# Optimization experiments

Hardware: AMD Instinct MI355X
Metric: run time of the kernel (lower is better)

## Reference

```python
import jax, jax.numpy as jnp
import numpy as np

B, T, D = 8, 1024, 768
H, HD = 12, 64
DFF = 3072
EPS = 1e-5


def setup_inputs() -> dict:
    key = jax.random.key(0)
    ks = jax.random.split(key, 6)
    s = lambda fan_in: 1.0 / np.sqrt(fan_in)
    return {
        "x": jax.random.normal(ks[0], (B, T, D), jnp.float32),
        "ln1_g": jnp.ones((D,), jnp.float32),
        "ln1_b": jnp.zeros((D,), jnp.float32),
        "w_qkv": jax.random.normal(ks[1], (D, 3 * D), jnp.float32) * s(D),
        "b_qkv": jnp.zeros((3 * D,), jnp.float32),
        "w_out": jax.random.normal(ks[2], (D, D), jnp.float32) * s(D),
        "b_out": jnp.zeros((D,), jnp.float32),
        "ln2_g": jnp.ones((D,), jnp.float32),
        "ln2_b": jnp.zeros((D,), jnp.float32),
        "w_fc1": jax.random.normal(ks[3], (D, DFF), jnp.float32) * s(D),
        "b_fc1": jnp.zeros((DFF,), jnp.float32),
        "w_fc2": jax.random.normal(ks[4], (DFF, D), jnp.float32) * s(DFF),
        "b_fc2": jnp.zeros((D,), jnp.float32),
    }


def _layernorm(x, g, b):
    mu = jnp.mean(x, axis=-1, keepdims=True)
    var = jnp.var(x, axis=-1, keepdims=True)
    return (x - mu) * jax.lax.rsqrt(var + EPS) * g + b


def reference(x, ln1_g, ln1_b, w_qkv, b_qkv, w_out, b_out,
              ln2_g, ln2_b, w_fc1, b_fc1, w_fc2, b_fc2):
    # --- attention branch (pre-norm) ---
    h = _layernorm(x, ln1_g, ln1_b)
    qkv = h @ w_qkv + b_qkv                      # [B,T,3D]
    q, k, v = jnp.split(qkv, 3, axis=-1)
    # [B,T,D] -> [B,H,T,HD]
    re = lambda t: t.reshape(B, T, H, HD).transpose(0, 2, 1, 3)
    q, k, v = re(q), re(k), re(v)
    scores = jnp.einsum("bhqd,bhkd->bhqk", q, k) * (1.0 / np.sqrt(HD))
    causal = jnp.tril(jnp.ones((T, T), bool))    # [T,T]
    scores = jnp.where(causal, scores, -jnp.inf)
    attn_weights = jax.nn.softmax(scores, axis=-1)  # [B,H,T,T]
    out = jnp.einsum("bhqk,bhkd->bhqd", attn_weights, v)
    out = out.transpose(0, 2, 1, 3).reshape(B, T, D)
    attn_out = out @ w_out + b_out
    x = x + attn_out
    # --- MLP branch (pre-norm) ---
    h2 = _layernorm(x, ln2_g, ln2_b)
    ff = jax.nn.gelu(h2 @ w_fc1 + b_fc1, approximate=False) @ w_fc2 + b_fc2
    x = x + ff
    return x, attn_weights
```

## Files before the change

kernel.cpp:

```cpp
#include <hip/hip_runtime.h>
#include <cstdint>
#include <cstddef>

namespace {

constexpr int Bb  = 8;
constexpr int Tt  = 1024;
constexpr int Dd  = 768;
constexpr int Hh  = 12;
constexpr int DFF = 3072;
constexpr int BT  = Bb * Tt;

typedef __attribute__((ext_vector_type(8))) short bf16x8;
typedef __attribute__((ext_vector_type(4))) short bf16x4;
typedef __attribute__((ext_vector_type(4))) float f32x4;

__device__ __forceinline__ short f2bf(float f) {
  union { float f; unsigned u; } v; v.f = f;
  unsigned r = v.u + 0x7fffu + ((v.u >> 16) & 1u);
  return (short)(r >> 16);
}
__device__ __forceinline__ float gelu_exact(float v) {
  return 0.5f * v * (1.0f + erff(v * 0.70710678118654752f));
}

#define MFMA16(a, b, c) __builtin_amdgcn_mfma_f32_16x16x32_bf16(a, b, c, 0, 0, 0)

__device__ __forceinline__ void gl_lds16(const short* g, short* l) {
  __builtin_amdgcn_global_load_lds(
      (const __attribute__((address_space(1))) unsigned int*)(g),
      (__attribute__((address_space(3))) unsigned int*)(l), 16, 0, 0);
}

__global__ __launch_bounds__(256) void cvt_t(const float* __restrict__ in,
                                             short* __restrict__ out,
                                             int K, int N) {
  __shared__ float tile[32][33];
  int k0 = blockIdx.x * 32, n0 = blockIdx.y * 32;
  int tx = threadIdx.x & 31, ty = threadIdx.x >> 5;
  #pragma unroll
  for (int r = ty; r < 32; r += 8)
    tile[r][tx] = in[(size_t)(k0 + r) * N + n0 + tx];
  __syncthreads();
  #pragma unroll
  for (int r = ty; r < 32; r += 8)
    out[(size_t)(n0 + r) * K + k0 + tx] = f2bf(tile[tx][r]);
}

__global__ __launch_bounds__(256) void ln_rows(const float* __restrict__ x,
                                               const float* __restrict__ g,
                                               const float* __restrict__ b,
                                               short* __restrict__ out) {
  int lane = threadIdx.x & 63, wid = threadIdx.x >> 6;
  int row = blockIdx.x * 4 + wid;
  const float* xr = x + (size_t)row * Dd;
  float v[12];
  float s = 0.f, ss = 0.f;
  #pragma unroll
  for (int c = 0; c < 3; c++) {
    float4 t = *(const float4*)&xr[c * 256 + lane * 4];
    v[c * 4 + 0] = t.x; v[c * 4 + 1] = t.y; v[c * 4 + 2] = t.z; v[c * 4 + 3] = t.w;
    s  += t.x + t.y + t.z + t.w;
    ss += t.x * t.x + t.y * t.y + t.z * t.z + t.w * t.w;
  }
  #pragma unroll
  for (int off = 1; off < 64; off <<= 1) {
    s += __shfl_xor(s, off); ss += __shfl_xor(ss, off);
  }
  float mu   = s * (1.f / Dd);
  float var  = ss * (1.f / Dd) - mu * mu;
  float rstd = rsqrtf(var + 1e-5f);
  #pragma unroll
  for (int c = 0; c < 3; c++) {
    bf16x4 o;
    #pragma unroll
    for (int j = 0; j < 4; j++) {
      int d = c * 256 + lane * 4 + j;
      o[j] = f2bf((v[c * 4 + j] - mu) * rstd * g[d] + b[d]);
    }
    *(bf16x4*)&out[(size_t)row * Dd + c * 256 + lane * 4] = o;
  }
}

__global__ __launch_bounds__(256) void vtr(const short* __restrict__ qkv,
                                           short* __restrict__ vt) {
  __shared__ short Ts[64][72];
  int bh = blockIdx.x, t0 = blockIdx.y * 64;
  int b = bh / Hh, h = bh % Hh;
  int tid = threadIdx.x;
  int r = tid >> 2, dc = (tid & 3) * 16;
  const short* vp = qkv + (size_t)b * Tt * 2304 + (size_t)(t0 + r) * 2304 + 1536 + h * 64 + dc;
  bf16x8 v0 = *(const bf16x8*)vp;
  bf16x8 v1 = *(const bf16x8*)(vp + 8);
  *(bf16x8*)&Ts[r][dc] = v0;
  *(bf16x8*)&Ts[r][dc + 8] = v1;
  __syncthreads();
  int d = tid >> 2, tc = (tid & 3) * 16;
  bf16x8 o0, o1;
  #pragma unroll
  for (int j = 0; j < 8; j++) { o0[j] = Ts[tc + j][d]; o1[j] = Ts[tc + 8 + j][d]; }
  short* op = vt + ((size_t)bh * 64 + d) * Tt + t0 + tc;
  *(bf16x8*)op = o0;
  *(bf16x8*)(op + 8) = o1;
}

template <int EPI, int N>
__global__ __launch_bounds__(256) void gemm_bt(const short* __restrict__ A,
                                               const short* __restrict__ Bt,
                                               const float* __restrict__ bias,
                                               const float* __restrict__ add,
                                               void* __restrict__ outp,
                                               int K) {
  __shared__ short S[17408];
  short* As0 = S;
  short* As1 = S + 4096;
  short* Bs0 = S + 8192;
  short* Bs1 = S + 12288;

  int nbx = gridDim.x;
  int flat = blockIdx.y * nbx + blockIdx.x;
  int cpx = (nbx * gridDim.y) >> 3;
  int swz = (flat & 7) * cpx + (flat >> 3);
  int m0 = (swz % nbx) * 128, n0 = (swz / nbx) * 128;

  int tid = threadIdx.x;
  int lane = tid & 63, wid = tid >> 6;
  int wm = wid >> 1, wn = wid & 1;
  int l15 = lane & 15, lg = lane >> 4;

  int jr = tid >> 2, jc = (tid & 3) << 3;
  int ldsb = wid << 9;

  auto stage = [&](short* Ad, short* Bd, int k0) {
    gl_lds16(&A[(size_t)(m0 + jr) * K + k0 + jc],       Ad + ldsb);
    gl_lds16(&A[(size_t)(m0 + 64 + jr) * K + k0 + jc],  Ad + 2048 + ldsb);
    gl_lds16(&Bt[(size_t)(n0 + jr) * K + k0 + jc],      Bd + ldsb);
    gl_lds16(&Bt[(size_t)(n0 + 64 + jr) * K + k0 + jc], Bd + 2048 + ldsb);
  };

  f32x4 acc[4][4] = {};
  stage(As0, Bs0, 0);
  int nk = K >> 5;
  for (int t = 0; t < nk; ++t) {
    short* Ab = (t & 1) ? As1 : As0;
    short* Bb = (t & 1) ? Bs1 : Bs0;
    if (t + 1 < nk) {
      stage((t & 1) ? As0 : As1, (t & 1) ? Bs0 : Bs1, (t + 1) << 5);
      asm volatile("s_waitcnt vmcnt(4)" ::: "memory");
    } else {
      asm volatile("s_waitcnt vmcnt(0)" ::: "memory");
    }
    __syncthreads();
    bf16x8 af[4], bfr[4];
    #pragma unroll
    for (int i = 0; i < 4; i++) af[i]  = *(bf16x8*)&Ab[(wm * 64 + i * 16 + l15) * 32 + lg * 8];
    #pragma unroll
    for (int j = 0; j < 4; j++) bfr[j] = *(bf16x8*)&Bb[(wn * 64 + j * 16 + l15) * 32 + lg * 8];
    #pragma unroll
    for (int i = 0; i < 4; i++)
      #pragma unroll
      for (int j = 0; j < 4; j++)
        acc[i][j] = MFMA16(af[i], bfr[j], acc[i][j]);
    __syncthreads();
  }

  if (EPI == 0 || EPI == 2) {
    short (*Cl)[136] = (short (*)[136])S;
    #pragma unroll
    for (int i = 0; i < 4; i++)
      #pragma unroll
      for (int j = 0; j < 4; j++)
        #pragma unroll
        for (int r = 0; r < 4; r++) {
          int row = wm * 64 + i * 16 + lg * 4 + r;
          int col = wn * 64 + j * 16 + l15;
          float vv = acc[i][j][r] + bias[n0 + col];
          if (EPI == 2) vv = gelu_exact(vv);
          int ch = col >> 3, co = col & 7;
          Cl[row][((ch ^ (row & 7)) << 3) | co] = f2bf(vv);
        }
    __syncthreads();
    int row = tid >> 1;
    int cb = (tid & 1) * 8;
    #pragma unroll
    for (int c = 0; c < 8; c++) {
      int ch = cb + c;
      bf16x8 v8 = *(bf16x8*)&Cl[row][(ch ^ (row & 7)) << 3];
      *(bf16x8*)&((short*)outp)[(size_t)(m0 + row) * N + n0 + (ch << 3)] = v8;
    }
  } else {
    #pragma unroll
    for (int i = 0; i < 4; i++)
      #pragma unroll
      for (int j = 0; j < 4; j++)
        #pragma unroll
        for (int r = 0; r < 4; r++) {
          int m = m0 + wm * 64 + i * 16 + lg * 4 + r;
          int n = n0 + wn * 64 + j * 16 + l15;
          float vv = acc[i][j][r] + bias[n];
          size_t idx = (size_t)m * N + n;
          float ov = vv + add[idx];
          if (EPI == 3) __builtin_nontemporal_store(ov, &((float*)outp)[idx]);
          else          ((float*)outp)[idx] = ov;
        }
  }
}

template <int EPI>
__global__ __launch_bounds__(256) void gemm_n64(const short* __restrict__ A,
                                                const short* __restrict__ Bt,
                                                const float* __restrict__ bias,
                                                const float* __restrict__ add,
                                                float* __restrict__ outp,
                                                int K) {
  constexpr int N = 768;
  __shared__ short S[12288];
  short* As0 = S;
  short* As1 = S + 2048;
  short* Bs0 = S + 4096;
  short* Bs1 = S + 8192;

  int nbx = gridDim.x;
  int flat = blockIdx.y * nbx + blockIdx.x;
  int cpx = (nbx * gridDim.y) >> 3;
  int swz = (flat & 7) * cpx + (flat >> 3);
  int m0 = (swz % nbx) * 64, n0 = (swz / nbx) * 128;

  int tid = threadIdx.x;
  int lane = tid & 63, wid = tid >> 6;
  int wm = wid & 1, wn = wid >> 1;
  int l15 = lane & 15, lg = lane >> 4;

  int jr = tid >> 2, jc = (tid & 3) << 3;
  int ldsb = wid << 9;

  auto stage = [&](short* Ad, short* Bd, int k0) {
    gl_lds16(&A[(size_t)(m0 + jr) * K + k0 + jc],       Ad + ldsb);
    gl_lds16(&Bt[(size_t)(n0 + jr) * K + k0 + jc],      Bd + ldsb);
    gl_lds16(&Bt[(size_t)(n0 + 64 + jr) * K + k0 + jc], Bd + 2048 + ldsb);
  };

  f32x4 acc[2][4] = {};
  stage(As0, Bs0, 0);
  int nk = K >> 5;
  for (int t = 0; t < nk; ++t) {
    short* Ab = (t & 1) ? As1 : As0;
    short* Bb = (t & 1) ? Bs1 : Bs0;
    if (t + 1 < nk) {
      stage((t & 1) ? As0 : As1, (t & 1) ? Bs0 : Bs1, (t + 1) << 5);
      asm volatile("s_waitcnt vmcnt(3)" ::: "memory");
    } else {
      asm volatile("s_waitcnt vmcnt(0)" ::: "memory");
    }
    __syncthreads();
    bf16x8 af[2], bfr[4];
    #pragma unroll
    for (int i = 0; i < 2; i++) af[i]  = *(bf16x8*)&Ab[(wm * 32 + i * 16 + l15) * 32 + lg * 8];
    #pragma unroll
    for (int j = 0; j < 4; j++) bfr[j] = *(bf16x8*)&Bb[(wn * 64 + j * 16 + l15) * 32 + lg * 8];
    #pragma unroll
    for (int i = 0; i < 2; i++)
      #pragma unroll
      for (int j = 0; j < 4; j++)
        acc[i][j] = MFMA16(af[i], bfr[j], acc[i][j]);
    __syncthreads();
  }

  #pragma unroll
  for (int i = 0; i < 2; i++)
    #pragma unroll
    for (int j = 0; j < 4; j++)
      #pragma unroll
      for (int r = 0; r < 4; r++) {
        int m = m0 + wm * 32 + i * 16 + lg * 4 + r;
        int n = n0 + wn * 64 + j * 16 + l15;
        float vv = acc[i][j][r] + bias[n];
        size_t idx = (size_t)m * N + n;
        float ov = vv + add[idx];
        if (EPI == 3) __builtin_nontemporal_store(ov, &outp[idx]);
        else          outp[idx] = ov;
      }
}

__global__ __launch_bounds__(256) void attn_fused(const short* __restrict__ qkv,
                                                  const short* __restrict__ vt,
                                                  float* __restrict__ attw,
                                                  short* __restrict__ ctx) {
  __shared__ short VtL[2][4096];
  __shared__ float Pf[4][16][68];
  int flat = blockIdx.y * 16 + blockIdx.x;
  int xcd = flat & 7, rr0 = flat >> 3;
  int bh   = xcd * 12 + (rr0 >> 4);
  int tile = 15 - (rr0 & 15);
  int q0 = tile * 64;
  int b = bh / Hh, h = bh % Hh;
  int tid = threadIdx.x, lane = tid & 63, wid = tid >> 6;
  int l15 = lane & 15, lg = lane >> 4;
  const short* base = qkv + (size_t)b * Tt * 2304;

  bf16x8 qa[2];
  {
    const short* qp = base + (size_t)(q0 + wid * 16 + l15) * 2304 + h * 64 + lg * 8;
    qa[0] = *(const bf16x8*)qp;
    qa[1] = *(const bf16x8*)(qp + 32);
  }

  float l[4] = {0.f, 0.f, 0.f, 0.f};
  for (int kt = 0; kt <= tile; ++kt) {
    f32x4 acc[4] = {};
    #pragma unroll
    for (int nf = 0; nf < 4; ++nf) {
      const short* kp = base + (size_t)(kt * 64 + nf * 16 + l15) * 2304 + 768 + h * 64 + lg * 8;
      bf16x8 k0 = *(const bf16x8*)kp;
      bf16x8 k1 = *(const bf16x8*)(kp + 32);
      acc[nf] = MFMA16(qa[0], k0, acc[nf]);
      acc[nf] = MFMA16(qa[1], k1, acc[nf]);
    }
    #pragma unroll
    for (int r = 0; r < 4; r++) {
      int qg = q0 + wid * 16 + lg * 4 + r;
      #pragma unroll
      for (int nf = 0; nf < 4; nf++) {
        int kg = kt * 64 + nf * 16 + l15;
        l[r] += (kg <= qg) ? __expf(acc[nf][r] * 0.125f) : 0.f;
      }
    }
  }
  float rl[4];
  #pragma unroll
  for (int r = 0; r < 4; r++) {
    float s = l[r];
    #pragma unroll
    for (int off = 1; off < 16; off <<= 1) s += __shfl_xor(s, off);
    rl[r] = 1.f / s;
  }

  const short* vtb = vt + (size_t)bh * 64 * Tt;
  int dS = wid * 16 + (lane >> 3);
  int cS = (lane & 7) ^ (lane >> 3);
  auto stageV = [&](int bi, int kt) {
    gl_lds16(&vtb[(size_t)dS * Tt + kt * 64 + cS * 8],       &VtL[bi][wid * 1024]);
    gl_lds16(&vtb[(size_t)(dS + 8) * Tt + kt * 64 + cS * 8], &VtL[bi][wid * 1024 + 512]);
  };

  f32x4 oacc[4] = {};
  stageV(0, 0);
  for (int kt = 0; kt <= tile; ++kt) {
    int cur = kt & 1;
    f32x4 acc[4] = {};
    #pragma unroll
    for (int nf = 0; nf < 4; nf++) {
      const short* kp = base + (size_t)(kt * 64 + nf * 16 + l15) * 2304 + 768 + h * 64 + lg * 8;
      bf16x8 k0 = *(const bf16x8*)kp;
      bf16x8 k1 = *(const bf16x8*)(kp + 32);
      acc[nf] = MFMA16(qa[0], k0, acc[nf]);
      acc[nf] = MFMA16(qa[1], k1, acc[nf]);
    }
    #pragma unroll
    for (int nf = 0; nf < 4; nf++) {
      #pragma unroll
      for (int r = 0; r < 4; r++) {
        int qg = q0 + wid * 16 + lg * 4 + r;
        int kg = kt * 64 + nf * 16 + l15;
        float p = (kg <= qg) ? __expf(acc[nf][r] * 0.125f) * rl[r] : 0.f;
        Pf[wid][lg * 4 + r][nf * 16 + l15] = p;
      }
    }
    asm volatile("s_waitcnt lgkmcnt(0)" ::: "memory");
    __builtin_amdgcn_sched_barrier(0);
    #pragma unroll
    for (int it = 0; it < 4; ++it) {
      int pr = it * 4 + lg;
      f32x4 pv = *(f32x4*)&Pf[wid][pr][l15 * 4];
      __builtin_nontemporal_store(
          pv, (f32x4*)&attw[((size_t)bh * Tt + q0 + wid * 16 + pr) * Tt + kt * 64 + l15 * 4]);
    }
    f32x4 pf0 = *(f32x4*)&Pf[wid][l15][lg * 8];
    f32x4 pf1 = *(f32x4*)&Pf[wid][l15][lg * 8 + 4];
    f32x4 pf2 = *(f32x4*)&Pf[wid][l15][lg * 8 + 32];
    f32x4 pf3 = *(f32x4*)&Pf[wid][l15][lg * 8 + 36];
    bf16x8 pa0, pa1;
    #pragma unroll
    for (int j = 0; j < 4; j++) {
      pa0[j] = f2bf(pf0[j]); pa0[4 + j] = f2bf(pf1[j]);
      pa1[j] = f2bf(pf2[j]); pa1[4 + j] = f2bf(pf3[j]);
    }
    asm volatile("s_waitcnt vmcnt(4)" ::: "memory");
    __builtin_amdgcn_s_barrier();
    __builtin_amdgcn_sched_barrier(0);
    if (kt < tile) stageV(cur ^ 1, kt + 1);
    #pragma unroll
    for (int nf = 0; nf < 4; nf++) {
      int dA = nf * 16 + l15;
      int sw = dA & 7;
      bf16x8 vb0 = *(bf16x8*)&VtL[cur][dA * 64 + ((lg ^ sw) << 3)];
      bf16x8 vb1 = *(bf16x8*)&VtL[cur][dA * 64 + (((4 + lg) ^ sw) << 3)];
      oacc[nf] = MFMA16(pa0, vb0, oacc[nf]);
      oacc[nf] = MFMA16(pa1, vb1, oacc[nf]);
    }
  }
  f32x4 z = {0.f, 0.f, 0.f, 0.f};
  for (int kt = tile + 1; kt < 16; ++kt) {
    #pragma unroll
    for (int it = 0; it < 4; ++it) {
      int pr = it * 4 + lg;
      __builtin_nontemporal_store(
          z, (f32x4*)&attw[((size_t)bh * Tt + q0 + wid * 16 + pr) * Tt + kt * 64 + l15 * 4]);
    }
  }
  #pragma unroll
  for (int nf = 0; nf < 4; nf++) {
    #pragma unroll
    for (int r = 0; r < 4; r++) {
      int t = q0 + wid * 16 + lg * 4 + r;
      ctx[((size_t)b * Tt + t) * Dd + h * 64 + nf * 16 + l15] = f2bf(oacc[nf][r]);
    }
  }
}

}

extern "C" void kernel_launch(void* const* d_in, const int* in_sizes, int n_in,
                              void* d_out, int out_size, void* d_ws, size_t ws_size,
                              hipStream_t stream) {
  const float* x     = (const float*)d_in[0];
  const float* ln1g  = (const float*)d_in[1];
  const float* ln1b  = (const float*)d_in[2];
  const float* w_qkv = (const float*)d_in[3];
  const float* b_qkv = (const float*)d_in[4];
  const float* w_out = (const float*)d_in[5];
  const float* b_out = (const float*)d_in[6];
  const float* ln2g  = (const float*)d_in[7];
  const float* ln2b  = (const float*)d_in[8];
  const float* w_fc1 = (const float*)d_in[9];
  const float* b_fc1 = (const float*)d_in[10];
  const float* w_fc2 = (const float*)d_in[11];
  const float* b_fc2 = (const float*)d_in[12];

  char* ws = (char*)d_ws;
  size_t o = 0;
  short* wqkvT = (short*)(ws + o); o += (size_t)2304 * 768 * 2;
  short* woutT = (short*)(ws + o); o += (size_t)768 * 768 * 2;
  short* wfc1T = (short*)(ws + o); o += (size_t)3072 * 768 * 2;
  short* wfc2T = (short*)(ws + o); o += (size_t)768 * 3072 * 2;
  short* h     = (short*)(ws + o); o += (size_t)BT * Dd * 2;
  short* qkv   = (short*)(ws + o); o += (size_t)BT * 2304 * 2;
  float* y1    = (float*)(ws + o); o += (size_t)BT * Dd * 4;
  short* h2    = (short*)(ws + o); o += (size_t)BT * Dd * 2;
  short* vt    = (short*)(ws + o); o += (size_t)96 * 64 * Tt * 2;
  short* ctx  = h;
  short* gbuf = h;

  float* out_x = (float*)d_out;
  float* attw  = out_x + (size_t)BT * Dd;

  cvt_t<<<dim3(768 / 32, 2304 / 32), 256, 0, stream>>>(w_qkv, wqkvT, 768, 2304);
  cvt_t<<<dim3(768 / 32, 768 / 32),  256, 0, stream>>>(w_out, woutT, 768, 768);
  cvt_t<<<dim3(768 / 32, 3072 / 32), 256, 0, stream>>>(w_fc1, wfc1T, 768, 3072);
  cvt_t<<<dim3(3072 / 32, 768 / 32), 256, 0, stream>>>(w_fc2, wfc2T, 3072, 768);

  ln_rows<<<BT / 4, 256, 0, stream>>>(x, ln1g, ln1b, h);
  gemm_bt<0, 2304><<<dim3(BT / 128, 2304 / 128), 256, 0, stream>>>(h, wqkvT, b_qkv, nullptr, qkv, 768);
  vtr<<<dim3(96, 16), 256, 0, stream>>>(qkv, vt);
  attn_fused<<<dim3(16, 96), 256, 0, stream>>>(qkv, vt, attw, ctx);
  gemm_n64<1><<<dim3(BT / 64, 768 / 128), 256, 0, stream>>>(ctx, woutT, b_out, x, y1, 768);
  ln_rows<<<BT / 4, 256, 0, stream>>>(y1, ln2g, ln2b, h2);
  gemm_bt<2, 3072><<<dim3(BT / 128, 3072 / 128), 256, 0, stream>>>(h2, wfc1T, b_fc1, nullptr, gbuf, 768);
  gemm_n64<3><<<dim3(BT / 64, 768 / 128), 256, 0, stream>>>(gbuf, wfc2T, b_fc2, y1, out_x, 3072);
}
```

Before: 432.9 us.

## Move causal-mask zeroing of attention weights into the QKV GEMM launch

Zeroing the upper-triangular attention-weight tiles is moved out of the fused attention kernel into a combined kernel that interleaves QKV GEMM blocks with zero-store blocks (3 GEMM blocks per 4 zeroing blocks). The goal is to overlap the store-bound zero writes with the compute-bound GEMM and to shorten the attention kernel's tail. The cost is a more complex block mapping, and the zero stores may compete with the GEMM for memory bandwidth.

```diff
diff --git a/kernel.cpp b/kernel.cpp
--- a/kernel.cpp
+++ b/kernel.cpp
@@ -104,23 +104,36 @@
   *(bf16x8*)(op + 8) = o1;
 }
 
+__device__ __forceinline__ void zero_block(int job, float* __restrict__ attw) {
+  int bh = job >> 4;
+  int tile = job & 15;
+  if (tile == 15) return;
+  int q0 = tile * 64;
+  int tid = threadIdx.x, lane = tid & 63, wid = tid >> 6;
+  int l15 = lane & 15, lg = lane >> 4;
+  f32x4 z = {0.f, 0.f, 0.f, 0.f};
+  for (int kt = tile + 1; kt < 16; ++kt) {
+    #pragma unroll
+    for (int it = 0; it < 4; ++it) {
+      int pr = wid * 16 + it * 4 + lg;
+      __builtin_nontemporal_store(
+          z, (f32x4*)&attw[((size_t)bh * Tt + q0 + pr) * Tt + kt * 64 + l15 * 4]);
+    }
+  }
+}
+
 template <int EPI, int N>
-__global__ __launch_bounds__(256) void gemm_bt(const short* __restrict__ A,
-                                               const short* __restrict__ Bt,
-                                               const float* __restrict__ bias,
-                                               const float* __restrict__ add,
-                                               void* __restrict__ outp,
-                                               int K) {
-  __shared__ short S[17408];
+__device__ __forceinline__ void gemm_block(short* S, int g, int cpx, int nbx,
+                                           const short* __restrict__ A,
+                                           const short* __restrict__ Bt,
+                                           const float* __restrict__ bias,
+                                           const float* __restrict__ add,
+                                           void* __restrict__ outp, int K) {
   short* As0 = S;
   short* As1 = S + 4096;
   short* Bs0 = S + 8192;
   short* Bs1 = S + 12288;
-
-  int nbx = gridDim.x;
-  int flat = blockIdx.y * nbx + blockIdx.x;
-  int cpx = (nbx * gridDim.y) >> 3;
-  int swz = (flat & 7) * cpx + (flat >> 3);
+  int swz = (g & 7) * cpx + (g >> 3);
   int m0 = (swz % nbx) * 128, n0 = (swz / nbx) * 128;
 
   int tid = threadIdx.x;
@@ -203,6 +216,37 @@
           if (EPI == 3) __builtin_nontemporal_store(ov, &((float*)outp)[idx]);
           else          ((float*)outp)[idx] = ov;
         }
+  }
+}
+
+template <int EPI, int N>
+__global__ __launch_bounds__(256) void gemm_bt(const short* __restrict__ A,
+                                               const short* __restrict__ Bt,
+                                               const float* __restrict__ bias,
+                                               const float* __restrict__ add,
+                                               void* __restrict__ outp,
+                                               int K) {
+  __shared__ short S[17408];
+  int nbx = gridDim.x;
+  int flat = blockIdx.y * nbx + blockIdx.x;
+  int cpx = (nbx * gridDim.y) >> 3;
+  gemm_block<EPI, N>(S, flat, cpx, nbx, A, Bt, bias, add, outp, K);
+}
+
+template <int EPI, int N, int GPG, int APG>
+__global__ __launch_bounds__(256) void gemm_mixz(const short* __restrict__ A,
+                                                 const short* __restrict__ Bt,
+                                                 const float* __restrict__ bias,
+                                                 void* __restrict__ outp, int K,
+                                                 int nbx, int cpx,
+                                                 float* __restrict__ attw) {
+  __shared__ short S[17408];
+  int bid = blockIdx.x;
+  int grp = bid / (GPG + APG), r = bid % (GPG + APG);
+  if (r < GPG) {
+    gemm_block<EPI, N>(S, grp * GPG + r, cpx, nbx, A, Bt, bias, nullptr, outp, K);
+  } else {
+    zero_block(grp * APG + (r - GPG), attw);
   }
 }
 
@@ -397,15 +441,6 @@
       bf16x8 vb1 = *(bf16x8*)&VtL[cur][dA * 64 + (((4 + lg) ^ sw) << 3)];
       oacc[nf] = MFMA16(pa0, vb0, oacc[nf]);
       oacc[nf] = MFMA16(pa1, vb1, oacc[nf]);
-    }
-  }
-  f32x4 z = {0.f, 0.f, 0.f, 0.f};
-  for (int kt = tile + 1; kt < 16; ++kt) {
-    #pragma unroll
-    for (int it = 0; it < 4; ++it) {
-      int pr = it * 4 + lg;
-      __builtin_nontemporal_store(
-          z, (f32x4*)&attw[((size_t)bh * Tt + q0 + wid * 16 + pr) * Tt + kt * 64 + l15 * 4]);
     }
   }
   #pragma unroll
@@ -460,7 +495,8 @@
   cvt_t<<<dim3(3072 / 32, 768 / 32), 256, 0, stream>>>(w_fc2, wfc2T, 3072, 768);
 
   ln_rows<<<BT / 4, 256, 0, stream>>>(x, ln1g, ln1b, h);
-  gemm_bt<0, 2304><<<dim3(BT / 128, 2304 / 128), 256, 0, stream>>>(h, wqkvT, b_qkv, nullptr, qkv, 768);
+  gemm_mixz<0, 2304, 3, 4><<<2688, 256, 0, stream>>>(
+      h, wqkvT, b_qkv, qkv, 768, BT / 128, 1152 / 8, attw);
   vtr<<<dim3(96, 16), 256, 0, stream>>>(qkv, vt);
   attn_fused<<<dim3(16, 96), 256, 0, stream>>>(qkv, vt, attw, ctx);
   gemm_n64<1><<<dim3(BT / 64, 768 / 128), 256, 0, stream>>>(ctx, woutT, b_out, x, y1, 768);
```

New measurement: 440.4 us. Within noise of the previous version (+1.7%).
